# Kernel tuning notes

Hardware: AMD Instinct MI355X
Metric: run time of the kernel (lower is better)

Reference implementation:

```python
import jax, jax.numpy as jnp
import numpy as np

B, G, N, E, F, H = 16, 8, 512, 8192, 128, 128
BN_EPS = 1e-5


def setup_inputs() -> dict:
    key = jax.random.key(0)
    ks = jax.random.split(key, 6)
    feats = jax.random.normal(ks[0], (B, G, N, F), jnp.float32)
    edges = jax.random.randint(ks[1], (B, G, 2, E), 0, N, dtype=jnp.int32)
    s = lambda k, shape: jax.random.normal(k, shape, jnp.float32) * 0.05
    return {
        "feats": feats,
        "edges": edges,
        "W0": s(ks[2], (F, H)), "b0": jnp.zeros((H,), jnp.float32),
        "W1": s(ks[3], (H, H)), "b1": jnp.zeros((H,), jnp.float32),
        "Wt": s(ks[4], (H, H)), "bt": jnp.zeros((H,), jnp.float32),
        "gamma": jnp.ones((H,), jnp.float32),
        "beta": jnp.zeros((H,), jnp.float32),
        "run_mean": jnp.zeros((H,), jnp.float32),
        "run_var": jnp.ones((H,), jnp.float32),
    }


def _gconv(x, src, dst, W, b):
    # DGL GraphConv with norm='both': relu(D_in^{-1/2} A D_out^{-1/2} X W + b)
    ones = jnp.ones(src.shape, jnp.float32)
    out_deg = jnp.clip(jax.ops.segment_sum(ones, src, num_segments=N), 1.0)
    in_deg = jnp.clip(jax.ops.segment_sum(ones, dst, num_segments=N), 1.0)
    h = x * jax.lax.rsqrt(out_deg)[:, None]          # src normalization
    agg = jax.ops.segment_sum(h[src], dst, num_segments=N)  # SpMM gather+scatter
    h = agg * jax.lax.rsqrt(in_deg)[:, None]          # dst normalization
    return jax.nn.relu(h @ W + b)


def reference(feats, edges, W0, b0, W1, b1, Wt, bt, gamma, beta, run_mean, run_var):
    def per_graph(x, e):
        src, dst = e[0], e[1]
        h = _gconv(x, src, dst, W0, b0)
        h = _gconv(h, src, dst, W1, b1)
        emb = h.mean(axis=0)  # dgl.mean_nodes readout -> [H]
        z = emb @ Wt + bt
        # BatchNorm1d in eval mode (batch of 1 graph embedding)
        z = gamma * (z - run_mean) * jax.lax.rsqrt(run_var + BN_EPS) + beta
        return jax.nn.relu(z)

    xf = feats.reshape(B * G, N, F)
    ef = edges.reshape(B * G, 2, E)
    out = jax.vmap(per_graph)(xf, ef)  # [B*G, H]
    # torch.stack nesting gives (batch, n_graph, 1, H) since mean_nodes returns [1, H]
    return out.reshape(B, G, 1, H)
```

## Files before the change

### kernel.cpp

```cpp
#include <hip/hip_runtime.h>
#include <hip/hip_bf16.h>

#define NN 512
#define NE 8192
#define NG 128
#define FH 128
#define APITCH 68
#define XPITCH 136
#define BN_EPS 1e-5f

typedef __attribute__((ext_vector_type(8))) short s8v;
typedef __attribute__((ext_vector_type(4))) float f4v;
typedef __attribute__((ext_vector_type(16))) float f16v;
typedef __attribute__((ext_vector_type(4))) unsigned short us4v;
typedef __attribute__((ext_vector_type(4))) unsigned int u4v;

__device__ inline unsigned short f2bf(float x) {
    unsigned u = __float_as_uint(x);
    unsigned r = (u + 0x7fffu + ((u >> 16) & 1u)) >> 16;
    return (unsigned short)r;
}
__device__ inline float bf2f(unsigned short h) { return __uint_as_float(((unsigned)h) << 16); }

__device__ inline unsigned bfpack(int f1bits, int f0bits) {
    return __builtin_amdgcn_perm((unsigned)f1bits, (unsigned)f0bits, 0x07060302u);
}

__device__ inline int aswz(int row, int col) {
    return row * APITCH + ((((col >> 2) ^ (((row >> 3) & 3) << 1)) << 2) | (col & 3));
}

__global__ __launch_bounds__(1024) void k_build(const int* __restrict__ edges,
                                                float* __restrict__ rs_out,
                                                float* __restrict__ rs_in,
                                                int* __restrict__ bofs,
                                                unsigned short* __restrict__ epk,
                                                const float* __restrict__ W0,
                                                const float* __restrict__ W1,
                                                unsigned short* __restrict__ WP) {
    int g = blockIdx.x;
    int tid = threadIdx.x;

    if (g >= NG) {
        int which = g - NG;
        const float* W = which ? W1 : W0;
        for (int task = tid; task < 2048; task += 1024) {
            int t = task >> 6;
            int lane = task & 63;
            int nt = t >> 2, kk = t & 3;
            int n = nt * 16 + (lane & 15);
            int k0 = kk * 32 + (lane >> 4) * 8;
            unsigned short* dh = WP + ((size_t)which * 2 + 0) * 16384 + ((size_t)t * 64 + lane) * 8;
            unsigned short* dl = WP + ((size_t)which * 2 + 1) * 16384 + ((size_t)t * 64 + lane) * 8;
#pragma unroll
            for (int j = 0; j < 8; j++) {
                float v = W[(size_t)(k0 + j) * FH + n];
                unsigned short h = f2bf(v);
                dh[j] = h;
                dl[j] = f2bf(v - bf2f(h));
            }
        }
        return;
    }

    const int* src = edges + (size_t)g * 2 * NE;
    const int* dst = src + NE;

    __shared__ int degO[NN], degI[NN];
    __shared__ int scanA[1024], scanB[1024];
    __shared__ int fill[1024];
    __shared__ unsigned short pk[NE];

    for (int i = tid; i < NN; i += 1024) { degO[i] = 0; degI[i] = 0; }
    scanA[tid] = 0;
    __syncthreads();

    int rep = tid & 31;
    for (int u = tid; u < NE / 4; u += 1024) {
        int4 s = ((const int4*)src)[u];
        int4 d = ((const int4*)dst)[u];
        atomicAdd(&degO[s.x], 1); atomicAdd(&degO[s.y], 1);
        atomicAdd(&degO[s.z], 1); atomicAdd(&degO[s.w], 1);
        atomicAdd(&degI[d.x], 1); atomicAdd(&degI[d.y], 1);
        atomicAdd(&degI[d.z], 1); atomicAdd(&degI[d.w], 1);
        atomicAdd(&scanA[((((d.x >> 7) << 3) | (s.x >> 6)) << 5) + rep], 1);
        atomicAdd(&scanA[((((d.y >> 7) << 3) | (s.y >> 6)) << 5) + rep], 1);
        atomicAdd(&scanA[((((d.z >> 7) << 3) | (s.z >> 6)) << 5) + rep], 1);
        atomicAdd(&scanA[((((d.w >> 7) << 3) | (s.w >> 6)) << 5) + rep], 1);
    }
    __syncthreads();

    for (int i = tid; i < NN; i += 1024) {
        rs_out[g * NN + i] = rsqrtf((float)max(degO[i], 1));
        rs_in [g * NN + i] = rsqrtf((float)max(degI[i], 1));
    }

    int* sA = scanA; int* sB = scanB;
    for (int off = 1; off < 1024; off <<= 1) {
        int v = sA[tid];
        if (tid >= off) v += sA[tid - off];
        sB[tid] = v;
        __syncthreads();
        int* t = sA; sA = sB; sB = t;
    }
    int excl = tid ? sA[tid - 1] : 0;
    fill[tid] = excl;
    if ((tid & 31) == 0) bofs[g * 33 + (tid >> 5)] = excl;
    if (tid == 0) bofs[g * 33 + 32] = NE;
    __syncthreads();

    for (int u = tid; u < NE / 4; u += 1024) {
        int4 s = ((const int4*)src)[u];
        int4 d = ((const int4*)dst)[u];
        int c, p;
        c = ((((d.x >> 7) << 3) | (s.x >> 6)) << 5) + rep;
        p = atomicAdd(&fill[c], 1); pk[p] = (unsigned short)(((d.x & 127) << 6) | (s.x & 63));
        c = ((((d.y >> 7) << 3) | (s.y >> 6)) << 5) + rep;
        p = atomicAdd(&fill[c], 1); pk[p] = (unsigned short)(((d.y & 127) << 6) | (s.y & 63));
        c = ((((d.z >> 7) << 3) | (s.z >> 6)) << 5) + rep;
        p = atomicAdd(&fill[c], 1); pk[p] = (unsigned short)(((d.z & 127) << 6) | (s.z & 63));
        c = ((((d.w >> 7) << 3) | (s.w >> 6)) << 5) + rep;
        p = atomicAdd(&fill[c], 1); pk[p] = (unsigned short)(((d.w & 127) << 6) | (s.w & 63));
    }
    __syncthreads();
    ((int4*)(epk + (size_t)g * NE))[tid] = ((const int4*)pk)[tid];
}

__global__ __launch_bounds__(256) void k_gemm_f32(const float* __restrict__ X,
                                                  const unsigned short* __restrict__ WPh,
                                                  const unsigned short* __restrict__ WPl,
                                                  const float* __restrict__ rs,
                                                  unsigned short* __restrict__ Yf) {
    __shared__ unsigned short xh[64 * XPITCH];
    __shared__ unsigned short xl[64 * XPITCH];
    int tid = threadIdx.x;
    int sb = blockIdx.y;
    size_t r0 = (size_t)blockIdx.x * NN + (size_t)sb * 64;

    const float4* Xv = (const float4*)(X + r0 * FH);
#pragma unroll
    for (int i = 0; i < 8; i++) {
        int u = tid + i * 256;
        int row = u >> 5, c4 = (u & 31) * 4;
        float4 v = Xv[u];
        int off = row * XPITCH + c4;
        unsigned short h0 = f2bf(v.x), h1 = f2bf(v.y), h2 = f2bf(v.z), h3 = f2bf(v.w);
        us4v hv, lv;
        hv.x = h0; hv.y = h1; hv.z = h2; hv.w = h3;
        lv.x = f2bf(v.x - bf2f(h0));
        lv.y = f2bf(v.y - bf2f(h1));
        lv.z = f2bf(v.z - bf2f(h2));
        lv.w = f2bf(v.w - bf2f(h3));
        *(us4v*)(xh + off) = hv;
        *(us4v*)(xl + off) = lv;
    }
    __syncthreads();

    int lane = tid & 63, w = tid >> 6;
    int quad = lane >> 4, m = lane & 15;
    int arow = w * 16 + m;

    f4v acc[8];
#pragma unroll
    for (int nt = 0; nt < 8; nt++) acc[nt] = (f4v){0.f, 0.f, 0.f, 0.f};

#pragma unroll
    for (int kk = 0; kk < 4; kk++) {
        s8v ah = *(const s8v*)&xh[arow * XPITCH + kk * 32 + quad * 8];
        s8v al = *(const s8v*)&xl[arow * XPITCH + kk * 32 + quad * 8];
#pragma unroll
        for (int nt = 0; nt < 8; nt++) {
            s8v bh = *(const s8v*)(WPh + ((size_t)(nt * 4 + kk) * 64 + lane) * 8);
            s8v bl = *(const s8v*)(WPl + ((size_t)(nt * 4 + kk) * 64 + lane) * 8);
            acc[nt] = __builtin_amdgcn_mfma_f32_16x16x32_bf16(ah, bh, acc[nt], 0, 0, 0);
            acc[nt] = __builtin_amdgcn_mfma_f32_16x16x32_bf16(al, bh, acc[nt], 0, 0, 0);
            acc[nt] = __builtin_amdgcn_mfma_f32_16x16x32_bf16(ah, bl, acc[nt], 0, 0, 0);
        }
    }

    int orow = w * 16 + quad * 4;
    float4 rsv = *(const float4*)(rs + r0 + orow);
    int kb = sb * 4 + w, h2 = quad >> 1, j0 = (quad & 1) * 4;
    unsigned short* of = Yf + (size_t)blockIdx.x * (NN * FH);
#pragma unroll
    for (int nt = 0; nt < 8; nt++) {
        us4v v;
        v.x = f2bf(acc[nt][0] * rsv.x);
        v.y = f2bf(acc[nt][1] * rsv.y);
        v.z = f2bf(acc[nt][2] * rsv.z);
        v.w = f2bf(acc[nt][3] * rsv.w);
        *(us4v*)(of + ((size_t)(kb * 2 + h2) * 128 + nt * 16 + m) * 8 + j0) = v;
    }
}

__global__ __launch_bounds__(512) void k_fused(const unsigned short* __restrict__ Y1f,
                                               const int* __restrict__ bofs,
                                               const unsigned short* __restrict__ epk,
                                               const float* __restrict__ rs_in,
                                               const float* __restrict__ rs_out,
                                               const float* __restrict__ bias,
                                               const unsigned short* __restrict__ WPh,
                                               const unsigned short* __restrict__ WPl,
                                               unsigned short* __restrict__ Y2f) {
    int g  = blockIdx.x;
    int sb = blockIdx.y;
    int tid = threadIdx.x;
    int lane = tid & 63, w8 = tid >> 6;
    int l31 = lane & 31, lh = lane >> 5;
    int mt = w8 & 3, nh = w8 >> 2;
    int base = sb * 128;

    __shared__ float Af[128 * APITCH];
    __shared__ unsigned short Bs[4 * 2 * 128 * 8];
    unsigned short* hs = (unsigned short*)Af;
    __shared__ float rsin_s[128];
    __shared__ int bo_s[9];

    const unsigned short* ep = epk + (size_t)g * NE;
    const int4* Yi4 = (const int4*)(Y1f + (size_t)g * (NN * FH));
    int4* Bi4 = (int4*)Bs;

    int4 rB0 = Yi4[tid];
    int4 rB1 = Yi4[tid + 512];

    if (tid < 128) rsin_s[tid] = rs_in[g * NN + base + tid];
    if (tid < 9) bo_s[tid] = bofs[g * 33 + sb * 8 + tid];
    __syncthreads();
    int evNext = -1;
    { int e0 = bo_s[0] + tid; if (e0 < bo_s[1]) evNext = (int)ep[e0]; }

    f16v acc32[2];
#pragma unroll
    for (int t = 0; t < 2; t++)
#pragma unroll
        for (int i = 0; i < 16; i++) acc32[t][i] = 0.f;

    for (int p = 0; p < 8; p++) {
        if (p) __syncthreads();
        float4 z4 = {0.f, 0.f, 0.f, 0.f};
        for (int i = tid; i < 128 * APITCH / 4; i += 512) ((float4*)Af)[i] = z4;
        Bi4[tid] = rB0;
        Bi4[tid + 512] = rB1;
        __syncthreads();
        if (evNext >= 0)
            atomicAdd(&Af[aswz(evNext >> 6, evNext & 63)], 1.0f);
        for (int e = bo_s[p] + tid + 512; e < bo_s[p + 1]; e += 512) {
            int v = ep[e];
            atomicAdd(&Af[aswz(v >> 6, v & 63)], 1.0f);
        }
        __syncthreads();
        if (p < 7) {
            rB0 = Yi4[(p + 1) * 1024 + tid];
            rB1 = Yi4[(p + 1) * 1024 + tid + 512];
            int e1 = bo_s[p + 1] + tid;
            evNext = (e1 < bo_s[p + 2]) ? (int)ep[e1] : -1;
        } else evNext = -1;
#pragma unroll
        for (int kk = 0; kk < 4; kk++) {
            s8v bf0 = *(const s8v*)&Bs[(((kk * 2 + lh) * 128) + nh * 64 + l31) * 8];
            s8v bf1 = *(const s8v*)&Bs[(((kk * 2 + lh) * 128) + nh * 64 + 32 + l31) * 8];
            int row = mt * 32 + l31;
            int chunk = (kk * 4 + lh * 2) ^ (((row >> 3) & 3) << 1);
            const int4* ap = (const int4*)&Af[row * APITCH + chunk * 4];
            int4 a0 = ap[0];
            int4 a1 = ap[1];
            union { u4v u; s8v s; } cv;
            cv.u.x = bfpack(a0.y, a0.x);
            cv.u.y = bfpack(a0.w, a0.z);
            cv.u.z = bfpack(a1.y, a1.x);
            cv.u.w = bfpack(a1.w, a1.z);
            acc32[0] = __builtin_amdgcn_mfma_f32_32x32x16_bf16(cv.s, bf0, acc32[0], 0, 0, 0);
            acc32[1] = __builtin_amdgcn_mfma_f32_32x32x16_bf16(cv.s, bf1, acc32[1], 0, 0, 0);
        }
    }
    __syncthreads();

#pragma unroll
    for (int t = 0; t < 2; t++) {
        int c = nh * 64 + t * 32 + l31;
        float bv = bias[c];
#pragma unroll
        for (int r = 0; r < 16; r++) {
            int row = mt * 32 + (r & 3) + 8 * (r >> 2) + 4 * lh;
            float hv = fmaxf(fmaf(rsin_s[row], acc32[t][r], bv), 0.f);
            hs[row * XPITCH + c] = f2bf(hv);
        }
    }
    __syncthreads();

    int quad = lane >> 4, m16 = lane & 15;
    f4v acc2[8];
#pragma unroll
    for (int nt = 0; nt < 8; nt++) acc2[nt] = (f4v){0.f, 0.f, 0.f, 0.f};

#pragma unroll
    for (int kk = 0; kk < 4; kk++) {
        s8v ah = *(const s8v*)&hs[(w8 * 16 + m16) * XPITCH + kk * 32 + quad * 8];
#pragma unroll
        for (int nt = 0; nt < 8; nt++) {
            s8v bh = *(const s8v*)(WPh + ((size_t)(nt * 4 + kk) * 64 + lane) * 8);
            s8v bl = *(const s8v*)(WPl + ((size_t)(nt * 4 + kk) * 64 + lane) * 8);
            acc2[nt] = __builtin_amdgcn_mfma_f32_16x16x32_bf16(ah, bh, acc2[nt], 0, 0, 0);
            acc2[nt] = __builtin_amdgcn_mfma_f32_16x16x32_bf16(ah, bl, acc2[nt], 0, 0, 0);
        }
    }

    int orow = w8 * 16 + quad * 4;
    float4 rsv = *(const float4*)(rs_out + (size_t)g * NN + base + orow);
    int kb = sb * 8 + w8, h2 = quad >> 1, j0 = (quad & 1) * 4;
    unsigned short* of = Y2f + (size_t)g * (NN * FH);
#pragma unroll
    for (int nt = 0; nt < 8; nt++) {
        us4v v;
        v.x = f2bf(acc2[nt][0] * rsv.x);
        v.y = f2bf(acc2[nt][1] * rsv.y);
        v.z = f2bf(acc2[nt][2] * rsv.z);
        v.w = f2bf(acc2[nt][3] * rsv.w);
        *(us4v*)(of + ((size_t)(kb * 2 + h2) * 128 + nt * 16 + m16) * 8 + j0) = v;
    }
}

__global__ __launch_bounds__(512) void k_gather_mean(const unsigned short* __restrict__ Y2f,
                                                     const int* __restrict__ bofs,
                                                     const unsigned short* __restrict__ epk,
                                                     const float* __restrict__ rs_in,
                                                     const float* __restrict__ bias,
                                                     float* __restrict__ partial) {
    int g  = blockIdx.x;
    int sb = blockIdx.y;
    int tid = threadIdx.x;
    int lane = tid & 63, w8 = tid >> 6;
    int l31 = lane & 31, lh = lane >> 5;
    int mt = w8 & 3, nh = w8 >> 2;
    int base = sb * 128;

    __shared__ float Af[128 * APITCH];
    __shared__ unsigned short Bs[4 * 2 * 128 * 8];
    float* red = (float*)Af;
    __shared__ float rsin_s[128];
    __shared__ int bo_s[9];

    const unsigned short* ep = epk + (size_t)g * NE;
    const int4* Yi4 = (const int4*)(Y2f + (size_t)g * (NN * FH));
    int4* Bi4 = (int4*)Bs;

    int4 rB0 = Yi4[tid];
    int4 rB1 = Yi4[tid + 512];

    if (tid < 128) rsin_s[tid] = rs_in[g * NN + base + tid];
    if (tid < 9) bo_s[tid] = bofs[g * 33 + sb * 8 + tid];
    __syncthreads();
    int evNext = -1;
    { int e0 = bo_s[0] + tid; if (e0 < bo_s[1]) evNext = (int)ep[e0]; }

    f16v acc32[2];
#pragma unroll
    for (int t = 0; t < 2; t++)
#pragma unroll
        for (int i = 0; i < 16; i++) acc32[t][i] = 0.f;

    for (int p = 0; p < 8; p++) {
        if (p) __syncthreads();
        float4 z4 = {0.f, 0.f, 0.f, 0.f};
        for (int i = tid; i < 128 * APITCH / 4; i += 512) ((float4*)Af)[i] = z4;
        Bi4[tid] = rB0;
        Bi4[tid + 512] = rB1;
        __syncthreads();
        if (evNext >= 0)
            atomicAdd(&Af[aswz(evNext >> 6, evNext & 63)], 1.0f);
        for (int e = bo_s[p] + tid + 512; e < bo_s[p + 1]; e += 512) {
            int v = ep[e];
            atomicAdd(&Af[aswz(v >> 6, v & 63)], 1.0f);
        }
        __syncthreads();
        if (p < 7) {
            rB0 = Yi4[(p + 1) * 1024 + tid];
            rB1 = Yi4[(p + 1) * 1024 + tid + 512];
            int e1 = bo_s[p + 1] + tid;
            evNext = (e1 < bo_s[p + 2]) ? (int)ep[e1] : -1;
        } else evNext = -1;
#pragma unroll
        for (int kk = 0; kk < 4; kk++) {
            s8v bf0 = *(const s8v*)&Bs[(((kk * 2 + lh) * 128) + nh * 64 + l31) * 8];
            s8v bf1 = *(const s8v*)&Bs[(((kk * 2 + lh) * 128) + nh * 64 + 32 + l31) * 8];
            int row = mt * 32 + l31;
            int chunk = (kk * 4 + lh * 2) ^ (((row >> 3) & 3) << 1);
            const int4* ap = (const int4*)&Af[row * APITCH + chunk * 4];
            int4 a0 = ap[0];
            int4 a1 = ap[1];
            union { u4v u; s8v s; } cv;
            cv.u.x = bfpack(a0.y, a0.x);
            cv.u.y = bfpack(a0.w, a0.z);
            cv.u.z = bfpack(a1.y, a1.x);
            cv.u.w = bfpack(a1.w, a1.z);
            acc32[0] = __builtin_amdgcn_mfma_f32_32x32x16_bf16(cv.s, bf0, acc32[0], 0, 0, 0);
            acc32[1] = __builtin_amdgcn_mfma_f32_32x32x16_bf16(cv.s, bf1, acc32[1], 0, 0, 0);
        }
    }
    __syncthreads();

#pragma unroll
    for (int t = 0; t < 2; t++) {
        int c = nh * 64 + t * 32 + l31;
        float bv = bias[c];
        float s = 0.f;
#pragma unroll
        for (int r = 0; r < 16; r++) {
            int row = mt * 32 + (r & 3) + 8 * (r >> 2) + 4 * lh;
            s += fmaxf(fmaf(rsin_s[row], acc32[t][r], bv), 0.f);
        }
        red[(w8 * 2 + t) * 64 + lane] = s;
    }
    __syncthreads();
    if (tid < FH) {
        int f = tid;
        int nh2 = f >> 6, t2 = (f >> 5) & 1, cl = f & 31;
        float t = 0.f;
#pragma unroll
        for (int mtt = 0; mtt < 4; mtt++) {
            int w = nh2 * 4 + mtt;
            t += red[(w * 2 + t2) * 64 + cl] + red[(w * 2 + t2) * 64 + cl + 32];
        }
        partial[((size_t)g * 4 + sb) * FH + f] = t;
    }
}

__global__ __launch_bounds__(128) void k_head(const float* __restrict__ partial,
                                              const float* __restrict__ Wt,
                                              const float* __restrict__ bt,
                                              const float* __restrict__ gamma,
                                              const float* __restrict__ beta,
                                              const float* __restrict__ rmean,
                                              const float* __restrict__ rvar,
                                              float* __restrict__ out) {
    int g = blockIdx.x;
    int j = threadIdx.x;
    __shared__ float e[FH];
    float acc4 = 0.f;
#pragma unroll
    for (int q = 0; q < 4; q++) acc4 += partial[((size_t)g * 4 + q) * FH + j];
    e[j] = acc4 * (1.0f / (float)NN);
    __syncthreads();
    float acc = bt[j];
#pragma unroll 8
    for (int k = 0; k < FH; k++) acc += e[k] * Wt[(size_t)k * FH + j];
    float z = gamma[j] * (acc - rmean[j]) * rsqrtf(rvar[j] + BN_EPS) + beta[j];
    out[g * FH + j] = fmaxf(z, 0.f);
}

extern "C" void kernel_launch(void* const* d_in, const int* in_sizes, int n_in,
                              void* d_out, int out_size, void* d_ws, size_t ws_size,
                              hipStream_t stream) {
    const float* feats = (const float*)d_in[0];
    const int*   edges = (const int*)d_in[1];
    const float* W0    = (const float*)d_in[2];
    const float* b0    = (const float*)d_in[3];
    const float* W1    = (const float*)d_in[4];
    const float* b1    = (const float*)d_in[5];
    const float* Wt    = (const float*)d_in[6];
    const float* bt    = (const float*)d_in[7];
    const float* gamma = (const float*)d_in[8];
    const float* beta  = (const float*)d_in[9];
    const float* rmean = (const float*)d_in[10];
    const float* rvar  = (const float*)d_in[11];
    float* out = (float*)d_out;

    char* w = (char*)d_ws;
    float* rs_out  = (float*)w;   w += sizeof(float) * NG * NN;
    float* rs_in   = (float*)w;   w += sizeof(float) * NG * NN;
    int*   bofs    = (int*)w;     w += sizeof(int) * NG * 33;
    unsigned short* epk = (unsigned short*)w; w += sizeof(unsigned short) * (size_t)NG * NE;
    unsigned short* WP  = (unsigned short*)w; w += sizeof(unsigned short) * 4 * 16384;
    unsigned short* Y1  = (unsigned short*)w; w += sizeof(unsigned short) * (size_t)NG * NN * FH;
    unsigned short* Y2  = (unsigned short*)w; w += sizeof(unsigned short) * (size_t)NG * NN * FH;
    float* partial = (float*)w;   w += sizeof(float) * NG * 4 * FH;

    unsigned short* WPh0 = WP;
    unsigned short* WPl0 = WP + 16384;
    unsigned short* WPh1 = WP + 32768;
    unsigned short* WPl1 = WP + 49152;

    k_build<<<NG + 2, 1024, 0, stream>>>(edges, rs_out, rs_in, bofs, epk, W0, W1, WP);

    k_gemm_f32<<<dim3(NG, 8), 256, 0, stream>>>(feats, WPh0, WPl0, rs_out, Y1);

    k_fused<<<dim3(NG, 4), 512, 0, stream>>>(Y1, bofs, epk, rs_in, rs_out, b0, WPh1, WPl1, Y2);

    k_gather_mean<<<dim3(NG, 4), 512, 0, stream>>>(Y2, bofs, epk, rs_in, b1, partial);

    k_head<<<NG, 128, 0, stream>>>(partial, Wt, bt, gamma, beta, rmean, rvar, out);

    (void)in_sizes; (void)n_in; (void)out_size; (void)ws_size;
}
```

Measured before the change: 169.7 us.

## Precompute dense bf16 adjacency tiles once and stream them into both aggregation GEMMs

Adds a k_packA kernel that builds each graph's dense adjacency count matrix from the bucketed edge list once, converts it to bf16, and stores it in global memory already laid out in MFMA fragment order. Previously both k_fused and k_gather_mean rebuilt the same adjacency with shared-memory atomics on every call. Both kernels now read A and Y fragments straight from global into registers with a double-buffered prefetch, which removes the LDS staging and the per-phase barriers. The cost is an extra 64 MB workspace buffer that is written once and read twice, plus one more kernel launch.

```diff
diff --git a/kernel.cpp b/kernel.cpp
--- a/kernel.cpp
+++ b/kernel.cpp
@@ -24,10 +24,6 @@
 
 __device__ inline unsigned bfpack(int f1bits, int f0bits) {
     return __builtin_amdgcn_perm((unsigned)f1bits, (unsigned)f0bits, 0x07060302u);
-}
-
-__device__ inline int aswz(int row, int col) {
-    return row * APITCH + ((((col >> 2) ^ (((row >> 3) & 3) << 1)) << 2) | (col & 3));
 }
 
 __global__ __launch_bounds__(1024) void k_build(const int* __restrict__ edges,
@@ -124,6 +120,50 @@
     }
     __syncthreads();
     ((int4*)(epk + (size_t)g * NE))[tid] = ((const int4*)pk)[tid];
+}
+
+__global__ __launch_bounds__(512) void k_packA(const int* __restrict__ bofs,
+                                               const unsigned short* __restrict__ epk,
+                                               unsigned short* __restrict__ AP) {
+    int g = blockIdx.x, sb = blockIdx.y, tid = threadIdx.x;
+    __shared__ float Af[128 * APITCH];
+    __shared__ int bo_s[9];
+    const unsigned short* ep = epk + (size_t)g * NE;
+    unsigned short* Ag = AP + (size_t)g * 262144;
+
+    if (tid < 9) bo_s[tid] = bofs[g * 33 + sb * 8 + tid];
+    __syncthreads();
+    int evNext = -1;
+    { int e0 = bo_s[0] + tid; if (e0 < bo_s[1]) evNext = (int)ep[e0]; }
+
+    for (int p = 0; p < 8; p++) {
+        if (p) __syncthreads();
+        float4 z4 = {0.f, 0.f, 0.f, 0.f};
+        for (int i = tid; i < 128 * APITCH / 4; i += 512) ((float4*)Af)[i] = z4;
+        __syncthreads();
+        if (evNext >= 0) atomicAdd(&Af[(evNext >> 6) * APITCH + (evNext & 63)], 1.0f);
+        for (int e = bo_s[p] + tid + 512; e < bo_s[p + 1]; e += 512) {
+            int v = ep[e];
+            atomicAdd(&Af[(v >> 6) * APITCH + (v & 63)], 1.0f);
+        }
+        __syncthreads();
+        if (p < 7) { int e1 = bo_s[p + 1] + tid; evNext = (e1 < bo_s[p + 2]) ? (int)ep[e1] : -1; }
+        else evNext = -1;
+#pragma unroll
+        for (int uu = 0; uu < 2; uu++) {
+            int u = tid + uu * 512;
+            int l31 = u & 31, lh = (u >> 5) & 1, Kl = (u >> 6) & 3, Rl = (u >> 8) & 3;
+            const int4* ap = (const int4*)&Af[(Rl * 32 + l31) * APITCH + Kl * 16 + lh * 8];
+            int4 a0 = ap[0], a1 = ap[1];
+            u4v cv;
+            cv.x = bfpack(a0.y, a0.x);
+            cv.y = bfpack(a0.w, a0.z);
+            cv.z = bfpack(a1.y, a1.x);
+            cv.w = bfpack(a1.w, a1.z);
+            int Rg = sb * 4 + Rl, K = p * 4 + Kl;
+            *(u4v*)(Ag + (((size_t)(Rg * 32 + K) * 2 + lh) * 32 + l31) * 8) = cv;
+        }
+    }
 }
 
 __global__ __launch_bounds__(256) void k_gemm_f32(const float* __restrict__ X,
@@ -194,8 +234,7 @@
 }
 
 __global__ __launch_bounds__(512) void k_fused(const unsigned short* __restrict__ Y1f,
-                                               const int* __restrict__ bofs,
-                                               const unsigned short* __restrict__ epk,
+                                               const unsigned short* __restrict__ AP,
                                                const float* __restrict__ rs_in,
                                                const float* __restrict__ rs_out,
                                                const float* __restrict__ bias,
@@ -210,24 +249,18 @@
     int mt = w8 & 3, nh = w8 >> 2;
     int base = sb * 128;
 
-    __shared__ float Af[128 * APITCH];
-    __shared__ unsigned short Bs[4 * 2 * 128 * 8];
-    unsigned short* hs = (unsigned short*)Af;
+    __shared__ unsigned short hs[128 * XPITCH];
     __shared__ float rsin_s[128];
-    __shared__ int bo_s[9];
-
-    const unsigned short* ep = epk + (size_t)g * NE;
-    const int4* Yi4 = (const int4*)(Y1f + (size_t)g * (NN * FH));
-    int4* Bi4 = (int4*)Bs;
-
-    int4 rB0 = Yi4[tid];
-    int4 rB1 = Yi4[tid + 512];
 
     if (tid < 128) rsin_s[tid] = rs_in[g * NN + base + tid];
-    if (tid < 9) bo_s[tid] = bofs[g * 33 + sb * 8 + tid];
-    __syncthreads();
-    int evNext = -1;
-    { int e0 = bo_s[0] + tid; if (e0 < bo_s[1]) evNext = (int)ep[e0]; }
+    __syncthreads();
+
+    const unsigned short* Yg = Y1f + (size_t)g * (NN * FH);
+    const unsigned short* Ag = AP + (size_t)g * 262144;
+    int Rg = sb * 4 + mt;
+    int aoff  = Rg * 16384 + lh * 256 + l31 * 8;
+    int boff0 = lh * 1024 + (nh * 64 + l31) * 8;
+    int boff1 = boff0 + 256;
 
     f16v acc32[2];
 #pragma unroll
@@ -235,45 +268,27 @@
 #pragma unroll
         for (int i = 0; i < 16; i++) acc32[t][i] = 0.f;
 
-    for (int p = 0; p < 8; p++) {
-        if (p) __syncthreads();
-        float4 z4 = {0.f, 0.f, 0.f, 0.f};
-        for (int i = tid; i < 128 * APITCH / 4; i += 512) ((float4*)Af)[i] = z4;
-        Bi4[tid] = rB0;
-        Bi4[tid + 512] = rB1;
-        __syncthreads();
-        if (evNext >= 0)
-            atomicAdd(&Af[aswz(evNext >> 6, evNext & 63)], 1.0f);
-        for (int e = bo_s[p] + tid + 512; e < bo_s[p + 1]; e += 512) {
-            int v = ep[e];
-            atomicAdd(&Af[aswz(v >> 6, v & 63)], 1.0f);
-        }
-        __syncthreads();
-        if (p < 7) {
-            rB0 = Yi4[(p + 1) * 1024 + tid];
-            rB1 = Yi4[(p + 1) * 1024 + tid + 512];
-            int e1 = bo_s[p + 1] + tid;
-            evNext = (e1 < bo_s[p + 2]) ? (int)ep[e1] : -1;
-        } else evNext = -1;
-#pragma unroll
-        for (int kk = 0; kk < 4; kk++) {
-            s8v bf0 = *(const s8v*)&Bs[(((kk * 2 + lh) * 128) + nh * 64 + l31) * 8];
-            s8v bf1 = *(const s8v*)&Bs[(((kk * 2 + lh) * 128) + nh * 64 + 32 + l31) * 8];
-            int row = mt * 32 + l31;
-            int chunk = (kk * 4 + lh * 2) ^ (((row >> 3) & 3) << 1);
-            const int4* ap = (const int4*)&Af[row * APITCH + chunk * 4];
-            int4 a0 = ap[0];
-            int4 a1 = ap[1];
-            union { u4v u; s8v s; } cv;
-            cv.u.x = bfpack(a0.y, a0.x);
-            cv.u.y = bfpack(a0.w, a0.z);
-            cv.u.z = bfpack(a1.y, a1.x);
-            cv.u.w = bfpack(a1.w, a1.z);
-            acc32[0] = __builtin_amdgcn_mfma_f32_32x32x16_bf16(cv.s, bf0, acc32[0], 0, 0, 0);
-            acc32[1] = __builtin_amdgcn_mfma_f32_32x32x16_bf16(cv.s, bf1, acc32[1], 0, 0, 0);
-        }
-    }
-    __syncthreads();
+    s8v aF[2][2], b0F[2][2], b1F[2][2];
+    auto LD = [&](int buf, int Kb) {
+#pragma unroll
+        for (int q = 0; q < 2; q++) {
+            int K = Kb + q;
+            aF[buf][q]  = *(const s8v*)(Ag + aoff  + K * 512);
+            b0F[buf][q] = *(const s8v*)(Yg + boff0 + K * 2048);
+            b1F[buf][q] = *(const s8v*)(Yg + boff1 + K * 2048);
+        }
+    };
+    LD(0, 0);
+#pragma unroll
+    for (int gq = 0; gq < 16; gq++) {
+        int cur = gq & 1;
+        if (gq < 15) LD(cur ^ 1, (gq + 1) * 2);
+#pragma unroll
+        for (int q = 0; q < 2; q++) {
+            acc32[0] = __builtin_amdgcn_mfma_f32_32x32x16_bf16(aF[cur][q], b0F[cur][q], acc32[0], 0, 0, 0);
+            acc32[1] = __builtin_amdgcn_mfma_f32_32x32x16_bf16(aF[cur][q], b1F[cur][q], acc32[1], 0, 0, 0);
+        }
+    }
 
 #pragma unroll
     for (int t = 0; t < 2; t++) {
@@ -321,8 +336,7 @@
 }
 
 __global__ __launch_bounds__(512) void k_gather_mean(const unsigned short* __restrict__ Y2f,
-                                                     const int* __restrict__ bofs,
-                                                     const unsigned short* __restrict__ epk,
+                                                     const unsigned short* __restrict__ AP,
                                                      const float* __restrict__ rs_in,
                                                      const float* __restrict__ bias,
                                                      float* __restrict__ partial) {
@@ -334,24 +348,18 @@
     int mt = w8 & 3, nh = w8 >> 2;
     int base = sb * 128;
 
-    __shared__ float Af[128 * APITCH];
-    __shared__ unsigned short Bs[4 * 2 * 128 * 8];
-    float* red = (float*)Af;
+    __shared__ float red[8 * 2 * 64];
     __shared__ float rsin_s[128];
-    __shared__ int bo_s[9];
-
-    const unsigned short* ep = epk + (size_t)g * NE;
-    const int4* Yi4 = (const int4*)(Y2f + (size_t)g * (NN * FH));
-    int4* Bi4 = (int4*)Bs;
-
-    int4 rB0 = Yi4[tid];
-    int4 rB1 = Yi4[tid + 512];
 
     if (tid < 128) rsin_s[tid] = rs_in[g * NN + base + tid];
-    if (tid < 9) bo_s[tid] = bofs[g * 33 + sb * 8 + tid];
-    __syncthreads();
-    int evNext = -1;
-    { int e0 = bo_s[0] + tid; if (e0 < bo_s[1]) evNext = (int)ep[e0]; }
+    __syncthreads();
+
+    const unsigned short* Yg = Y2f + (size_t)g * (NN * FH);
+    const unsigned short* Ag = AP + (size_t)g * 262144;
+    int Rg = sb * 4 + mt;
+    int aoff  = Rg * 16384 + lh * 256 + l31 * 8;
+    int boff0 = lh * 1024 + (nh * 64 + l31) * 8;
+    int boff1 = boff0 + 256;
 
     f16v acc32[2];
 #pragma unroll
@@ -359,45 +367,27 @@
 #pragma unroll
         for (int i = 0; i < 16; i++) acc32[t][i] = 0.f;
 
-    for (int p = 0; p < 8; p++) {
-        if (p) __syncthreads();
-        float4 z4 = {0.f, 0.f, 0.f, 0.f};
-        for (int i = tid; i < 128 * APITCH / 4; i += 512) ((float4*)Af)[i] = z4;
-        Bi4[tid] = rB0;
-        Bi4[tid + 512] = rB1;
-        __syncthreads();
-        if (evNext >= 0)
-            atomicAdd(&Af[aswz(evNext >> 6, evNext & 63)], 1.0f);
-        for (int e = bo_s[p] + tid + 512; e < bo_s[p + 1]; e += 512) {
-            int v = ep[e];
-            atomicAdd(&Af[aswz(v >> 6, v & 63)], 1.0f);
-        }
-        __syncthreads();
-        if (p < 7) {
-            rB0 = Yi4[(p + 1) * 1024 + tid];
-            rB1 = Yi4[(p + 1) * 1024 + tid + 512];
-            int e1 = bo_s[p + 1] + tid;
-            evNext = (e1 < bo_s[p + 2]) ? (int)ep[e1] : -1;
-        } else evNext = -1;
-#pragma unroll
-        for (int kk = 0; kk < 4; kk++) {
-            s8v bf0 = *(const s8v*)&Bs[(((kk * 2 + lh) * 128) + nh * 64 + l31) * 8];
-            s8v bf1 = *(const s8v*)&Bs[(((kk * 2 + lh) * 128) + nh * 64 + 32 + l31) * 8];
-            int row = mt * 32 + l31;
-            int chunk = (kk * 4 + lh * 2) ^ (((row >> 3) & 3) << 1);
-            const int4* ap = (const int4*)&Af[row * APITCH + chunk * 4];
-            int4 a0 = ap[0];
-            int4 a1 = ap[1];
-            union { u4v u; s8v s; } cv;
-            cv.u.x = bfpack(a0.y, a0.x);
-            cv.u.y = bfpack(a0.w, a0.z);
-            cv.u.z = bfpack(a1.y, a1.x);
-            cv.u.w = bfpack(a1.w, a1.z);
-            acc32[0] = __builtin_amdgcn_mfma_f32_32x32x16_bf16(cv.s, bf0, acc32[0], 0, 0, 0);
-            acc32[1] = __builtin_amdgcn_mfma_f32_32x32x16_bf16(cv.s, bf1, acc32[1], 0, 0, 0);
-        }
-    }
-    __syncthreads();
+    s8v aF[2][2], b0F[2][2], b1F[2][2];
+    auto LD = [&](int buf, int Kb) {
+#pragma unroll
+        for (int q = 0; q < 2; q++) {
+            int K = Kb + q;
+            aF[buf][q]  = *(const s8v*)(Ag + aoff  + K * 512);
+            b0F[buf][q] = *(const s8v*)(Yg + boff0 + K * 2048);
+            b1F[buf][q] = *(const s8v*)(Yg + boff1 + K * 2048);
+        }
+    };
+    LD(0, 0);
+#pragma unroll
+    for (int gq = 0; gq < 16; gq++) {
+        int cur = gq & 1;
+        if (gq < 15) LD(cur ^ 1, (gq + 1) * 2);
+#pragma unroll
+        for (int q = 0; q < 2; q++) {
+            acc32[0] = __builtin_amdgcn_mfma_f32_32x32x16_bf16(aF[cur][q], b0F[cur][q], acc32[0], 0, 0, 0);
+            acc32[1] = __builtin_amdgcn_mfma_f32_32x32x16_bf16(aF[cur][q], b1F[cur][q], acc32[1], 0, 0, 0);
+        }
+    }
 
 #pragma unroll
     for (int t = 0; t < 2; t++) {
@@ -473,6 +463,7 @@
     unsigned short* WP  = (unsigned short*)w; w += sizeof(unsigned short) * 4 * 16384;
     unsigned short* Y1  = (unsigned short*)w; w += sizeof(unsigned short) * (size_t)NG * NN * FH;
     unsigned short* Y2  = (unsigned short*)w; w += sizeof(unsigned short) * (size_t)NG * NN * FH;
+    unsigned short* AP  = (unsigned short*)w; w += sizeof(unsigned short) * (size_t)NG * 262144;
     float* partial = (float*)w;   w += sizeof(float) * NG * 4 * FH;
 
     unsigned short* WPh0 = WP;
@@ -482,11 +473,13 @@
 
     k_build<<<NG + 2, 1024, 0, stream>>>(edges, rs_out, rs_in, bofs, epk, W0, W1, WP);
 
+    k_packA<<<dim3(NG, 4), 512, 0, stream>>>(bofs, epk, AP);
+
     k_gemm_f32<<<dim3(NG, 8), 256, 0, stream>>>(feats, WPh0, WPl0, rs_out, Y1);
 
-    k_fused<<<dim3(NG, 4), 512, 0, stream>>>(Y1, bofs, epk, rs_in, rs_out, b0, WPh1, WPl1, Y2);
-
-    k_gather_mean<<<dim3(NG, 4), 512, 0, stream>>>(Y2, bofs, epk, rs_in, b1, partial);
+    k_fused<<<dim3(NG, 4), 512, 0, stream>>>(Y1, AP, rs_in, rs_out, b0, WPh1, WPl1, Y2);
+
+    k_gather_mean<<<dim3(NG, 4), 512, 0, stream>>>(Y2, AP, rs_in, b1, partial);
 
     k_head<<<NG, 128, 0, stream>>>(partial, Wt, bt, gamma, beta, rmean, rvar, out);
 
```

New measurement: 185.3 us. 1.09x slower.
